# Kernel tuning notes

Measured on AMD Instinct MI355X. Metric: run time of the kernel, lower is better.

Reference implementation:

```python
import jax, jax.numpy as jnp
import numpy as np

B, N_ROIS, C, H, W = 4, 180, 512, 48, 48
STRIDE = 4
EPS = 1e-5


def _pool_one(feat, roi):
    # feat: [C,H,W], roi: [4] float (y1,x1,y2,x2) in image coords
    r = roi / STRIDE
    r0 = jnp.trunc(r[0]).astype(jnp.int32)
    r1 = jnp.trunc(r[1]).astype(jnp.int32)
    r2 = jnp.ceil(r[2]).astype(jnp.int32)
    r3 = jnp.ceil(r[3]).astype(jnp.int32)
    h_size = r2 - r0 + 1
    w_size = r3 - r1 + 1
    idx2 = jnp.arange(2)
    # AdaptiveMaxPool2d region boundaries: [floor(i*s/2), ceil((i+1)*s/2))
    sh = (idx2 * h_size) // 2
    eh = ((idx2 + 1) * h_size + 1) // 2
    sw = (idx2 * w_size) // 2
    ew = ((idx2 + 1) * w_size + 1) // 2
    hh = jnp.arange(H)[None, :]
    ww = jnp.arange(W)[None, :]
    mask_h = (hh >= (r0 + sh)[:, None]) & (hh < (r0 + eh)[:, None])  # [2,H]
    mask_w = (ww >= (r1 + sw)[:, None]) & (ww < (r1 + ew)[:, None])  # [2,W]
    neg = jnp.finfo(feat.dtype).min
    # max over W within each col region -> [2(oj), C, H]
    mw = jnp.where(mask_w[:, None, None, :], feat[None], neg).max(axis=-1)
    # max over H within each row region -> [2(oi), 2(oj), C]
    p = jnp.where(mask_h[:, None, None, :], mw[None], neg).max(axis=-1)
    # torch layout: [C, oi, oj] then flatten row-major
    return jnp.transpose(p, (2, 0, 1)).reshape(-1)  # [C*4]


def _roi_pool(features, rois):
    # features: [B,C,H,W], rois: [B,N,4] -> [B,N,C*4]
    def per_roi(roi_b):  # roi_b: [B,4]
        return jax.vmap(_pool_one)(features, roi_b)  # [B, C*4]
    out = jax.lax.map(per_roi, jnp.swapaxes(rois, 0, 1))  # [N,B,C*4]
    return jnp.swapaxes(out, 0, 1)


def _bn(x, gamma, beta):
    # training-mode BatchNorm1d over [B, N_ROIS(channels), F]: stats over (B,F)
    mean = x.mean(axis=(0, 2), keepdims=True)
    var = ((x - mean) ** 2).mean(axis=(0, 2), keepdims=True)
    return (x - mean) * jax.lax.rsqrt(var + EPS) * gamma[None, :, None] + beta[None, :, None]


def setup_inputs() -> dict:
    key = jax.random.key(0)
    k1, k2, k3, k4, k5 = jax.random.split(key, 5)
    features = jax.random.normal(k1, (B, C, H, W), dtype=jnp.float32)
    max_coord = (H - 1) * STRIDE
    y = jnp.sort(jax.random.uniform(k2, (B, N_ROIS, 2), minval=0.0, maxval=max_coord), axis=-1)
    x = jnp.sort(jax.random.uniform(k3, (B, N_ROIS, 2), minval=0.0, maxval=max_coord), axis=-1)
    rois = jnp.stack([y[..., 0], x[..., 0], y[..., 1], x[..., 1]], axis=-1)  # [B,N,4]
    F_in = C * 4
    W1 = jax.random.normal(k4, (64, F_in), dtype=jnp.float32) * 0.02
    bl1 = jnp.zeros((64,), dtype=jnp.float32)
    gamma1 = jnp.ones((N_ROIS,), dtype=jnp.float32)
    beta1 = jnp.zeros((N_ROIS,), dtype=jnp.float32)
    gamma2 = jnp.ones((N_ROIS,), dtype=jnp.float32)
    beta2 = jnp.zeros((N_ROIS,), dtype=jnp.float32)
    return {"features": features, "rois": rois, "gamma1": gamma1, "beta1": beta1,
            "W1": W1, "bl1": bl1, "gamma2": gamma2, "beta2": beta2}


def reference(features, rois, gamma1, beta1, W1, bl1, gamma2, beta2):
    pooled = _roi_pool(features, rois)            # [B, 180, 2048]
    x = jax.nn.relu(pooled)
    x = _bn(x, gamma1, beta1)
    y = jnp.einsum('bnf,of->bno', x, W1) + bl1    # [B, 180, 64]
    y = _bn(y, gamma2, beta2)
    return y
```

## Files before the change

kernel.cpp:

```cpp
#include <hip/hip_runtime.h>
#include <hip/hip_bf16.h>
#include <cfloat>
#include <math.h>

#define BB 4
#define NR 180
#define CC 512
#define HH 48
#define WW 48
#define FF (CC*4)
#define OO 64
#define EPSV 1e-5f
#define TW_LEVEL ((size_t)BB*HH*WW*CC)


typedef unsigned short us2 __attribute__((ext_vector_type(2)));

__device__ __forceinline__ unsigned pmax(unsigned a, unsigned b) {
    return __builtin_bit_cast(unsigned, __builtin_elementwise_max(
        __builtin_bit_cast(us2, a), __builtin_bit_cast(us2, b)));
}
__device__ __forceinline__ uint4 pmax4(uint4 a, uint4 b) {
    return make_uint4(pmax(a.x,b.x), pmax(a.y,b.y), pmax(a.z,b.z), pmax(a.w,b.w));
}
__device__ __forceinline__ unsigned mapb(float f) {
    unsigned fu = __float_as_uint(f);
    unsigned u = fu >> 16;
    return (fu >> 31) ? (~u & 0xFFFFu) : (u | 0x8000u);
}
__device__ __forceinline__ void unmap2(unsigned m, float& lo, float& hi) {
    unsigned t = ((~m) >> 15) & 0x00010001u;
    unsigned u = m ^ (0x80008000u ^ (t * 0x7FFFu));
    lo = __uint_as_float(u << 16);
    hi = __uint_as_float(u & 0xffff0000u);
}

__global__ __launch_bounds__(256) void k_prep(const float* __restrict__ feat,
                                              const float* __restrict__ W1,
                                              ushort* __restrict__ featB,
                                              float* __restrict__ W1T4) {
    __shared__ float tile[32][33];
    int t = threadIdx.x;
    int z = blockIdx.z;

    if (z < 4) {
        const int S = HH * WW;
        int b  = z;
        int s0 = blockIdx.x * 32;
        int c0 = blockIdx.y * 32;
        const float* src = feat + (size_t)b * CC * S;
        ushort* dst = featB + (size_t)b * S * CC;

        int cl = t >> 3;
        int sx = (t & 7) << 2;
        float4 v = *(const float4*)(src + (size_t)(c0 + cl) * S + s0 + sx);
        tile[cl][sx] = v.x; tile[cl][sx+1] = v.y; tile[cl][sx+2] = v.z; tile[cl][sx+3] = v.w;
        __syncthreads();

        int sl = t >> 3;
        int c4 = (t & 7) << 2;
        unsigned u0 = mapb(tile[c4][sl])   | (mapb(tile[c4+1][sl]) << 16);
        unsigned u1 = mapb(tile[c4+2][sl]) | (mapb(tile[c4+3][sl]) << 16);
        *(uint2*)(dst + (size_t)(s0 + sl) * CC + c0 + c4) = make_uint2(u0, u1);
    } else {
        if (blockIdx.x >= 8) return;
        int kt = blockIdx.y * 8 + blockIdx.x;
        int k0 = (kt >> 1) * 32, o0 = (kt & 1) * 32;
        int tx = t & 31, ty = t >> 5;
        #pragma unroll
        for (int k = 0; k < 4; k++) {
            int row = ty + k * 8;
            tile[row][tx] = W1[(size_t)(o0 + row) * FF + (k0 + tx)];
        }
        __syncthreads();
        #pragma unroll
        for (int k = 0; k < 4; k++) {
            int row = ty + k * 8;
            int kk = k0 + row;
            int o  = o0 + tx;
            W1T4[(size_t)(kk >> 2) * 256 + o * 4 + (kk & 3)] = tile[tx][row];
        }
    }
}

__global__ __launch_bounds__(256) void k_tab(const ushort* __restrict__ featB,
                                             ushort* __restrict__ Tw) {
    __shared__ uint4 A[WW][64];
    int by = blockIdx.x;
    int b = by / HH, y = by % HH;
    int t = threadIdx.x;
    const uint4* src = (const uint4*)(featB + (size_t)((b * HH + y) * WW) * CC);

    #pragma unroll
    for (int i = 0; i < 12; i++) {
        int it = t + i * 256;
        A[it >> 6][it & 63] = src[it];
    }
    __syncthreads();

    for (int k = 1; k <= 3; k++) {
        int h = 1 << (k - 1);
        uint4 v[12];
        #pragma unroll
        for (int i = 0; i < 12; i++) {
            int it = t + i * 256;
            int x = it >> 6, c = it & 63;
            v[i] = pmax4(A[x][c], A[min(x + h, WW - 1)][c]);
        }
        __syncthreads();
        if (k >= 2) {
            uint4* dst = (uint4*)(Tw + ((size_t)(k - 2) * BB * HH + b * HH + y) * (size_t)(WW * CC));
            #pragma unroll
            for (int i = 0; i < 12; i++) {
                int it = t + i * 256;
                A[it >> 6][it & 63] = v[i];
                dst[it] = v[i];
            }
        } else {
            #pragma unroll
            for (int i = 0; i < 12; i++) {
                int it = t + i * 256;
                A[it >> 6][it & 63] = v[i];
            }
        }
        __syncthreads();
    }
}

__global__ __launch_bounds__(1024) void k_pg(const ushort* __restrict__ featB,
                                             const ushort* __restrict__ Tw,
                                             const float* __restrict__ rois,
                                             const float* __restrict__ W1T4,
                                             const float* __restrict__ bl1,
                                             const float* __restrict__ g1,
                                             const float* __restrict__ b1,
                                             const float* __restrict__ g2,
                                             const float* __restrict__ b2,
                                             float* __restrict__ out) {
    __shared__ unsigned lu[BB][4][16][65];
    __shared__ float xs[BB][FF];
    __shared__ float pd[16][BB][OO];
    __shared__ float pw[16][OO];
    __shared__ float part_s[16], part_q[16];
    __shared__ float sm2[4], sq2[4];

    int n = blockIdx.x;
    int tid = threadIdx.x;
    int b  = tid >> 8;
    int g  = (tid >> 6) & 3;
    int c  = tid & 63;

    const float* roi = rois + ((size_t)b * NR + n) * 4;
    int r0 = (int)(roi[0] * 0.25f);
    int r1 = (int)(roi[1] * 0.25f);
    int r2 = (int)ceilf(roi[2] * 0.25f);
    int r3 = (int)ceilf(roi[3] * 0.25f);
    int hs  = r2 - r0 + 1;
    int wsz = r3 - r1 + 1;
    int eh0 = (hs + 1) >> 1, sh1 = hs >> 1;
    int sw1 = wsz >> 1;

    int len = (wsz + 1) >> 1;
    int ks  = (len >= 8) ? 3 : ((len >= 4) ? 2 : 0);
    int w   = 1 << ks;
    bool n3 = (len > 2 * w);
    int xboff = (len >> 1) - (w >> 1);
    int x0a = r1,        x0c = r1 + len - w,  x0b = r1 + xboff;
    int x1a = r1 + sw1,  x1c = r1 + wsz - w,  x1b = r1 + sw1 + xboff;
    const ushort* base = (ks == 0) ? featB : (Tw + (size_t)(ks - 2) * TW_LEVEL);

    const uint4 Z = make_uint4(0,0,0,0);
    uint4 q00 = Z, q01 = Z, q10 = Z, q11 = Z;
    for (int L = g; L < hs; L += 4) {
        size_t rowoff = (size_t)((b * HH + r0 + L) * WW) * CC;
        const uint4* p = (const uint4*)(base + rowoff) + c;
        uint4 cm0 = pmax4(p[(size_t)64 * x0a], p[(size_t)64 * x0c]);
        uint4 cm1 = pmax4(p[(size_t)64 * x1a], p[(size_t)64 * x1c]);
        if (n3) {
            cm0 = pmax4(cm0, p[(size_t)64 * x0b]);
            cm1 = pmax4(cm1, p[(size_t)64 * x1b]);
        }
        if (L <  eh0) { q00 = pmax4(q00, cm0); q01 = pmax4(q01, cm1); }
        if (L >= sh1) { q10 = pmax4(q10, cm0); q11 = pmax4(q11, cm1); }
    }

    {
        unsigned* L0 = &lu[b][g][0][c];
        unsigned a, p2;
        a = q00.x; p2 = q01.x;
        L0[ 0*65] = (a & 0xFFFFu) | (p2 << 16);
        L0[ 2*65] = (a >> 16)     | (p2 & 0xFFFF0000u);
        a = q10.x; p2 = q11.x;
        L0[ 1*65] = (a & 0xFFFFu) | (p2 << 16);
        L0[ 3*65] = (a >> 16)     | (p2 & 0xFFFF0000u);
        a = q00.y; p2 = q01.y;
        L0[ 4*65] = (a & 0xFFFFu) | (p2 << 16);
        L0[ 6*65] = (a >> 16)     | (p2 & 0xFFFF0000u);
        a = q10.y; p2 = q11.y;
        L0[ 5*65] = (a & 0xFFFFu) | (p2 << 16);
        L0[ 7*65] = (a >> 16)     | (p2 & 0xFFFF0000u);
        a = q00.z; p2 = q01.z;
        L0[ 8*65] = (a & 0xFFFFu) | (p2 << 16);
        L0[10*65] = (a >> 16)     | (p2 & 0xFFFF0000u);
        a = q10.z; p2 = q11.z;
        L0[ 9*65] = (a & 0xFFFFu) | (p2 << 16);
        L0[11*65] = (a >> 16)     | (p2 & 0xFFFF0000u);
        a = q00.w; p2 = q01.w;
        L0[12*65] = (a & 0xFFFFu) | (p2 << 16);
        L0[14*65] = (a >> 16)     | (p2 & 0xFFFF0000u);
        a = q10.w; p2 = q11.w;
        L0[13*65] = (a & 0xFFFFu) | (p2 << 16);
        L0[15*65] = (a >> 16)     | (p2 & 0xFFFF0000u);
    }
    __syncthreads();

    float s_acc = 0.f, q_acc = 0.f;
    int s  = tid & 255;
    int bb = tid >> 8;
    #pragma unroll
    for (int p = 0; p < 2; p++) {
        int fb = (p << 10) + (s << 2);
        int cc = fb >> 5;
        int j0 = (fb >> 1) & 15;
        unsigned m0 = pmax(pmax(lu[bb][0][j0  ][cc], lu[bb][1][j0  ][cc]),
                           pmax(lu[bb][2][j0  ][cc], lu[bb][3][j0  ][cc]));
        unsigned m1 = pmax(pmax(lu[bb][0][j0+1][cc], lu[bb][1][j0+1][cc]),
                           pmax(lu[bb][2][j0+1][cc], lu[bb][3][j0+1][cc]));
        m0 = pmax(m0, 0x80008000u);
        m1 = pmax(m1, 0x80008000u);
        float v0, v1, v2, v3;
        unmap2(m0, v0, v1);
        unmap2(m1, v2, v3);
        *(float4*)&xs[bb][fb] = make_float4(v0, v1, v2, v3);
        s_acc += v0 + v1 + v2 + v3;
        q_acc += v0*v0 + v1*v1 + v2*v2 + v3*v3;
    }
    for (int off = 32; off; off >>= 1) {
        s_acc += __shfl_down(s_acc, off);
        q_acc += __shfl_down(q_acc, off);
    }
    if ((tid & 63) == 0) { part_s[tid >> 6] = s_acc; part_q[tid >> 6] = q_acc; }
    __syncthreads();
    float ts = 0.f, tq = 0.f;
    #pragma unroll
    for (int i = 0; i < 16; i++) { ts += part_s[i]; tq += part_q[i]; }
    const float inv1 = 1.f / (float)(BB * FF);
    float mean = ts * inv1;
    float var  = tq * inv1 - mean * mean;
    float a1n  = g1[n] * rsqrtf(var + EPSV);
    float c1n  = b1[n] - mean * a1n;

    int sc = tid >> 6;
    int o  = tid & 63;
    int k4a = sc << 5;
    float a0 = 0.f, a1 = 0.f, a2 = 0.f, a3 = 0.f, wsum = 0.f;
    #pragma unroll 4
    for (int k4 = k4a; k4 < k4a + 32; k4++) {
        float4 w4 = *(const float4*)(W1T4 + (size_t)k4 * 256 + o * 4);
        float4 x0 = *(const float4*)&xs[0][k4 << 2];
        float4 x1 = *(const float4*)&xs[1][k4 << 2];
        float4 x2 = *(const float4*)&xs[2][k4 << 2];
        float4 x3 = *(const float4*)&xs[3][k4 << 2];
        wsum += w4.x + w4.y + w4.z + w4.w;
        a0 += w4.x*x0.x + w4.y*x0.y + w4.z*x0.z + w4.w*x0.w;
        a1 += w4.x*x1.x + w4.y*x1.y + w4.z*x1.z + w4.w*x1.w;
        a2 += w4.x*x2.x + w4.y*x2.y + w4.z*x2.z + w4.w*x2.w;
        a3 += w4.x*x3.x + w4.y*x3.y + w4.z*x3.z + w4.w*x3.w;
    }
    pd[sc][0][o] = a0; pd[sc][1][o] = a1; pd[sc][2][o] = a2; pd[sc][3][o] = a3;
    pw[sc][o] = wsum;
    __syncthreads();

    float y = 0.f;
    int bo = tid >> 6;
    if (tid < 256) {
        float dot = 0.f, wsm = 0.f;
        #pragma unroll
        for (int ss = 0; ss < 16; ss++) { dot += pd[ss][bo][o]; wsm += pw[ss][o]; }
        y = a1n * dot + c1n * wsm + bl1[o];
        float rs = y, rq = y * y;
        for (int off = 32; off; off >>= 1) {
            rs += __shfl_down(rs, off);
            rq += __shfl_down(rq, off);
        }
        if (o == 0) { sm2[bo] = rs; sq2[bo] = rq; }
    }
    __syncthreads();
    if (tid < 256) {
        float sm  = sm2[0] + sm2[1] + sm2[2] + sm2[3];
        float sqm = sq2[0] + sq2[1] + sq2[2] + sq2[3];
        const float inv2 = 1.f / 256.f;
        float mean2 = sm * inv2;
        float var2  = sqm * inv2 - mean2 * mean2;
        float r2s = rsqrtf(var2 + EPSV);
        out[((size_t)bo * NR + n) * OO + o] = (y - mean2) * r2s * g2[n] + b2[n];
    }
}

extern "C" void kernel_launch(void* const* d_in, const int* in_sizes, int n_in,
                              void* d_out, int out_size, void* d_ws, size_t ws_size,
                              hipStream_t stream) {
    const float* feat = (const float*)d_in[0];
    const float* rois = (const float*)d_in[1];
    const float* g1   = (const float*)d_in[2];
    const float* b1   = (const float*)d_in[3];
    const float* W1   = (const float*)d_in[4];
    const float* bl1  = (const float*)d_in[5];
    const float* g2   = (const float*)d_in[6];
    const float* b2   = (const float*)d_in[7];
    float* out = (float*)d_out;

    ushort* featB = (ushort*)d_ws;
    float*  W1T4  = (float*)(featB + (size_t)BB*HH*WW*CC);
    ushort* Tw    = (ushort*)(W1T4 + (size_t)OO*FF);

    k_prep<<<dim3(72, 16, 5), 256, 0, stream>>>(feat, W1, featB, W1T4);
    k_tab<<<dim3(BB * HH), 256, 0, stream>>>(featB, Tw);
    k_pg<<<dim3(NR), 1024, 0, stream>>>(featB, Tw, rois, W1T4, bl1, g1, b1, g2, b2, out);
}
```

Before: 110.4 us.

## Fuse prep, table and pooling kernels into one persistent kernel with grid barriers

Replaces the three launches (layout/bf16 conversion with W1 transpose, the sliding-max table build, and pooling plus linear plus BN) with one persistent 192-block kernel. Phases are separated by a software grid barrier built from per-block flag slots in the workspace, and shared memory is unioned across phases. This removes inter-kernel launch gaps and tail drain. In exchange, the prep phase has far fewer blocks, all blocks must be co-resident, and the barrier flags are never reset. A later call in the same workspace could therefore pass both barriers without waiting.

```diff
diff --git a/kernel.cpp b/kernel.cpp
--- a/kernel.cpp
+++ b/kernel.cpp
@@ -12,6 +12,9 @@
 #define OO 64
 #define EPSV 1e-5f
 #define TW_LEVEL ((size_t)BB*HH*WW*CC)
+#define NBLK 192
+#define MAGIC1 0xA5C3F00Du
+#define MAGIC2 0x5A3CF11Eu
 
 
 typedef unsigned short us2 __attribute__((ext_vector_type(2)));
@@ -35,117 +38,145 @@
     hi = __uint_as_float(u & 0xffff0000u);
 }
 
-__global__ __launch_bounds__(256) void k_prep(const float* __restrict__ feat,
-                                              const float* __restrict__ W1,
-                                              ushort* __restrict__ featB,
-                                              float* __restrict__ W1T4) {
-    __shared__ float tile[32][33];
-    int t = threadIdx.x;
-    int z = blockIdx.z;
-
-    if (z < 4) {
+union SmemT {
+    float tileA[4][32][33];
+    uint4 rowA[WW][64];
+    struct {
+        unsigned lu[BB][4][16][65];
+        float xs[BB][FF];
+        float pd[16][BB][OO];
+        float pw[16][OO];
+        float part_s[16], part_q[16];
+        float sm2[4], sq2[4];
+    } pg;
+};
+
+__device__ __forceinline__ void grid_barrier(unsigned* slots, unsigned magic,
+                                             int bid, int tid) {
+    __syncthreads();
+    if (tid == 0) {
+        __threadfence();
+        __hip_atomic_store(slots + bid, magic, __ATOMIC_RELEASE,
+                           __HIP_MEMORY_SCOPE_AGENT);
+    }
+    if (tid < NBLK) {
+        while (__hip_atomic_load(slots + tid, __ATOMIC_RELAXED,
+                                 __HIP_MEMORY_SCOPE_AGENT) != magic)
+            __builtin_amdgcn_s_sleep(1);
+    }
+    __syncthreads();
+    __threadfence();
+}
+
+__global__ __launch_bounds__(1024) void k_fused(
+        const float* __restrict__ feat, const float* __restrict__ rois,
+        const float* __restrict__ W1,
+        ushort* __restrict__ featB, float* __restrict__ W1T4,
+        ushort* __restrict__ Tw, unsigned* __restrict__ bar,
+        const float* __restrict__ bl1,
+        const float* __restrict__ g1, const float* __restrict__ b1,
+        const float* __restrict__ g2, const float* __restrict__ b2,
+        float* __restrict__ out) {
+    __shared__ SmemT sm;
+    int bid = blockIdx.x;
+    int tid = threadIdx.x;
+
+    {
+        int sub = tid >> 8;
+        int t   = tid & 255;
+        float (*tile)[33] = sm.tileA[sub];
         const int S = HH * WW;
-        int b  = z;
-        int s0 = blockIdx.x * 32;
-        int c0 = blockIdx.y * 32;
-        const float* src = feat + (size_t)b * CC * S;
-        ushort* dst = featB + (size_t)b * S * CC;
-
-        int cl = t >> 3;
-        int sx = (t & 7) << 2;
-        float4 v = *(const float4*)(src + (size_t)(c0 + cl) * S + s0 + sx);
-        tile[cl][sx] = v.x; tile[cl][sx+1] = v.y; tile[cl][sx+2] = v.z; tile[cl][sx+3] = v.w;
+        #pragma unroll 1
+        for (int i = 0; i < 6; i++) {
+            int u   = (bid * 4 + sub) * 6 + i;
+            int b   = u / 1152;
+            int rem = u - b * 1152;
+            int c0  = (rem / 72) * 32;
+            int s0  = (rem % 72) * 32;
+            const float* src = feat + (size_t)b * CC * S;
+            ushort* dst = featB + (size_t)b * S * CC;
+
+            int cl = t >> 3;
+            int sx = (t & 7) << 2;
+            float4 v = *(const float4*)(src + (size_t)(c0 + cl) * S + s0 + sx);
+            tile[cl][sx] = v.x; tile[cl][sx+1] = v.y;
+            tile[cl][sx+2] = v.z; tile[cl][sx+3] = v.w;
+            __syncthreads();
+            int sl = t >> 3;
+            int c4 = (t & 7) << 2;
+            unsigned u0 = mapb(tile[c4][sl])   | (mapb(tile[c4+1][sl]) << 16);
+            unsigned u1 = mapb(tile[c4+2][sl]) | (mapb(tile[c4+3][sl]) << 16);
+            *(uint2*)(dst + (size_t)(s0 + sl) * CC + c0 + c4) = make_uint2(u0, u1);
+            __syncthreads();
+        }
+        if (bid >= 184) {
+            #pragma unroll 1
+            for (int j = 0; j < 4; j++) {
+                int kt = (bid - 184) * 16 + sub * 4 + j;
+                int k0 = (kt >> 1) * 32, o0 = (kt & 1) * 32;
+                int tx = t & 31, ty = t >> 5;
+                #pragma unroll
+                for (int k = 0; k < 4; k++) {
+                    int row = ty + k * 8;
+                    tile[row][tx] = W1[(size_t)(o0 + row) * FF + (k0 + tx)];
+                }
+                __syncthreads();
+                #pragma unroll
+                for (int k = 0; k < 4; k++) {
+                    int row = ty + k * 8;
+                    int kk = k0 + row;
+                    int o  = o0 + tx;
+                    W1T4[(size_t)(kk >> 2) * 256 + o * 4 + (kk & 3)] = tile[tx][row];
+                }
+                __syncthreads();
+            }
+        }
+    }
+
+    grid_barrier(bar, MAGIC1, bid, tid);
+
+    {
+        int b = bid / HH, y = bid - b * HH;
+        const uint4* src = (const uint4*)(featB + (size_t)((b * HH + y) * WW) * CC);
+        #pragma unroll
+        for (int i = 0; i < 3; i++) {
+            int it = tid + i * 1024;
+            sm.rowA[it >> 6][it & 63] = src[it];
+        }
         __syncthreads();
-
-        int sl = t >> 3;
-        int c4 = (t & 7) << 2;
-        unsigned u0 = mapb(tile[c4][sl])   | (mapb(tile[c4+1][sl]) << 16);
-        unsigned u1 = mapb(tile[c4+2][sl]) | (mapb(tile[c4+3][sl]) << 16);
-        *(uint2*)(dst + (size_t)(s0 + sl) * CC + c0 + c4) = make_uint2(u0, u1);
-    } else {
-        if (blockIdx.x >= 8) return;
-        int kt = blockIdx.y * 8 + blockIdx.x;
-        int k0 = (kt >> 1) * 32, o0 = (kt & 1) * 32;
-        int tx = t & 31, ty = t >> 5;
-        #pragma unroll
-        for (int k = 0; k < 4; k++) {
-            int row = ty + k * 8;
-            tile[row][tx] = W1[(size_t)(o0 + row) * FF + (k0 + tx)];
-        }
-        __syncthreads();
-        #pragma unroll
-        for (int k = 0; k < 4; k++) {
-            int row = ty + k * 8;
-            int kk = k0 + row;
-            int o  = o0 + tx;
-            W1T4[(size_t)(kk >> 2) * 256 + o * 4 + (kk & 3)] = tile[tx][row];
-        }
-    }
-}
-
-__global__ __launch_bounds__(256) void k_tab(const ushort* __restrict__ featB,
-                                             ushort* __restrict__ Tw) {
-    __shared__ uint4 A[WW][64];
-    int by = blockIdx.x;
-    int b = by / HH, y = by % HH;
-    int t = threadIdx.x;
-    const uint4* src = (const uint4*)(featB + (size_t)((b * HH + y) * WW) * CC);
-
-    #pragma unroll
-    for (int i = 0; i < 12; i++) {
-        int it = t + i * 256;
-        A[it >> 6][it & 63] = src[it];
-    }
-    __syncthreads();
-
-    for (int k = 1; k <= 3; k++) {
-        int h = 1 << (k - 1);
-        uint4 v[12];
-        #pragma unroll
-        for (int i = 0; i < 12; i++) {
-            int it = t + i * 256;
-            int x = it >> 6, c = it & 63;
-            v[i] = pmax4(A[x][c], A[min(x + h, WW - 1)][c]);
-        }
-        __syncthreads();
-        if (k >= 2) {
-            uint4* dst = (uint4*)(Tw + ((size_t)(k - 2) * BB * HH + b * HH + y) * (size_t)(WW * CC));
+        for (int k = 1; k <= 3; k++) {
+            int h = 1 << (k - 1);
+            uint4 v[3];
             #pragma unroll
-            for (int i = 0; i < 12; i++) {
-                int it = t + i * 256;
-                A[it >> 6][it & 63] = v[i];
-                dst[it] = v[i];
+            for (int i = 0; i < 3; i++) {
+                int it = tid + i * 1024;
+                int x = it >> 6, c = it & 63;
+                v[i] = pmax4(sm.rowA[x][c], sm.rowA[min(x + h, WW - 1)][c]);
             }
-        } else {
-            #pragma unroll
-            for (int i = 0; i < 12; i++) {
-                int it = t + i * 256;
-                A[it >> 6][it & 63] = v[i];
+            __syncthreads();
+            if (k >= 2) {
+                uint4* dst = (uint4*)(Tw + ((size_t)(k - 2) * BB * HH + b * HH + y) * (size_t)(WW * CC));
+                #pragma unroll
+                for (int i = 0; i < 3; i++) {
+                    int it = tid + i * 1024;
+                    sm.rowA[it >> 6][it & 63] = v[i];
+                    dst[it] = v[i];
+                }
+            } else {
+                #pragma unroll
+                for (int i = 0; i < 3; i++) {
+                    int it = tid + i * 1024;
+                    sm.rowA[it >> 6][it & 63] = v[i];
+                }
             }
-        }
-        __syncthreads();
-    }
-}
-
-__global__ __launch_bounds__(1024) void k_pg(const ushort* __restrict__ featB,
-                                             const ushort* __restrict__ Tw,
-                                             const float* __restrict__ rois,
-                                             const float* __restrict__ W1T4,
-                                             const float* __restrict__ bl1,
-                                             const float* __restrict__ g1,
-                                             const float* __restrict__ b1,
-                                             const float* __restrict__ g2,
-                                             const float* __restrict__ b2,
-                                             float* __restrict__ out) {
-    __shared__ unsigned lu[BB][4][16][65];
-    __shared__ float xs[BB][FF];
-    __shared__ float pd[16][BB][OO];
-    __shared__ float pw[16][OO];
-    __shared__ float part_s[16], part_q[16];
-    __shared__ float sm2[4], sq2[4];
-
-    int n = blockIdx.x;
-    int tid = threadIdx.x;
+            __syncthreads();
+        }
+    }
+
+    grid_barrier(bar + 256, MAGIC2, bid, tid);
+    if (bid >= NR) return;
+
+    int n = bid;
     int b  = tid >> 8;
     int g  = (tid >> 6) & 3;
     int c  = tid & 63;
@@ -185,7 +216,7 @@
     }
 
     {
-        unsigned* L0 = &lu[b][g][0][c];
+        unsigned* L0 = &sm.pg.lu[b][g][0][c];
         unsigned a, p2;
         a = q00.x; p2 = q01.x;
         L0[ 0*65] = (a & 0xFFFFu) | (p2 << 16);
@@ -222,16 +253,16 @@
         int fb = (p << 10) + (s << 2);
         int cc = fb >> 5;
         int j0 = (fb >> 1) & 15;
-        unsigned m0 = pmax(pmax(lu[bb][0][j0  ][cc], lu[bb][1][j0  ][cc]),
-                           pmax(lu[bb][2][j0  ][cc], lu[bb][3][j0  ][cc]));
-        unsigned m1 = pmax(pmax(lu[bb][0][j0+1][cc], lu[bb][1][j0+1][cc]),
-                           pmax(lu[bb][2][j0+1][cc], lu[bb][3][j0+1][cc]));
+        unsigned m0 = pmax(pmax(sm.pg.lu[bb][0][j0  ][cc], sm.pg.lu[bb][1][j0  ][cc]),
+                           pmax(sm.pg.lu[bb][2][j0  ][cc], sm.pg.lu[bb][3][j0  ][cc]));
+        unsigned m1 = pmax(pmax(sm.pg.lu[bb][0][j0+1][cc], sm.pg.lu[bb][1][j0+1][cc]),
+                           pmax(sm.pg.lu[bb][2][j0+1][cc], sm.pg.lu[bb][3][j0+1][cc]));
         m0 = pmax(m0, 0x80008000u);
         m1 = pmax(m1, 0x80008000u);
         float v0, v1, v2, v3;
         unmap2(m0, v0, v1);
         unmap2(m1, v2, v3);
-        *(float4*)&xs[bb][fb] = make_float4(v0, v1, v2, v3);
+        *(float4*)&sm.pg.xs[bb][fb] = make_float4(v0, v1, v2, v3);
         s_acc += v0 + v1 + v2 + v3;
         q_acc += v0*v0 + v1*v1 + v2*v2 + v3*v3;
     }
@@ -239,11 +270,11 @@
         s_acc += __shfl_down(s_acc, off);
         q_acc += __shfl_down(q_acc, off);
     }
-    if ((tid & 63) == 0) { part_s[tid >> 6] = s_acc; part_q[tid >> 6] = q_acc; }
+    if ((tid & 63) == 0) { sm.pg.part_s[tid >> 6] = s_acc; sm.pg.part_q[tid >> 6] = q_acc; }
     __syncthreads();
     float ts = 0.f, tq = 0.f;
     #pragma unroll
-    for (int i = 0; i < 16; i++) { ts += part_s[i]; tq += part_q[i]; }
+    for (int i = 0; i < 16; i++) { ts += sm.pg.part_s[i]; tq += sm.pg.part_q[i]; }
     const float inv1 = 1.f / (float)(BB * FF);
     float mean = ts * inv1;
     float var  = tq * inv1 - mean * mean;
@@ -257,18 +288,19 @@
     #pragma unroll 4
     for (int k4 = k4a; k4 < k4a + 32; k4++) {
         float4 w4 = *(const float4*)(W1T4 + (size_t)k4 * 256 + o * 4);
-        float4 x0 = *(const float4*)&xs[0][k4 << 2];
-        float4 x1 = *(const float4*)&xs[1][k4 << 2];
-        float4 x2 = *(const float4*)&xs[2][k4 << 2];
-        float4 x3 = *(const float4*)&xs[3][k4 << 2];
+        float4 x0 = *(const float4*)&sm.pg.xs[0][k4 << 2];
+        float4 x1 = *(const float4*)&sm.pg.xs[1][k4 << 2];
+        float4 x2 = *(const float4*)&sm.pg.xs[2][k4 << 2];
+        float4 x3 = *(const float4*)&sm.pg.xs[3][k4 << 2];
         wsum += w4.x + w4.y + w4.z + w4.w;
         a0 += w4.x*x0.x + w4.y*x0.y + w4.z*x0.z + w4.w*x0.w;
         a1 += w4.x*x1.x + w4.y*x1.y + w4.z*x1.z + w4.w*x1.w;
         a2 += w4.x*x2.x + w4.y*x2.y + w4.z*x2.z + w4.w*x2.w;
         a3 += w4.x*x3.x + w4.y*x3.y + w4.z*x3.z + w4.w*x3.w;
     }
-    pd[sc][0][o] = a0; pd[sc][1][o] = a1; pd[sc][2][o] = a2; pd[sc][3][o] = a3;
-    pw[sc][o] = wsum;
+    sm.pg.pd[sc][0][o] = a0; sm.pg.pd[sc][1][o] = a1;
+    sm.pg.pd[sc][2][o] = a2; sm.pg.pd[sc][3][o] = a3;
+    sm.pg.pw[sc][o] = wsum;
     __syncthreads();
 
     float y = 0.f;
@@ -276,21 +308,21 @@
     if (tid < 256) {
         float dot = 0.f, wsm = 0.f;
         #pragma unroll
-        for (int ss = 0; ss < 16; ss++) { dot += pd[ss][bo][o]; wsm += pw[ss][o]; }
+        for (int ss = 0; ss < 16; ss++) { dot += sm.pg.pd[ss][bo][o]; wsm += sm.pg.pw[ss][o]; }
         y = a1n * dot + c1n * wsm + bl1[o];
         float rs = y, rq = y * y;
         for (int off = 32; off; off >>= 1) {
             rs += __shfl_down(rs, off);
             rq += __shfl_down(rq, off);
         }
-        if (o == 0) { sm2[bo] = rs; sq2[bo] = rq; }
+        if (o == 0) { sm.pg.sm2[bo] = rs; sm.pg.sq2[bo] = rq; }
     }
     __syncthreads();
     if (tid < 256) {
-        float sm  = sm2[0] + sm2[1] + sm2[2] + sm2[3];
-        float sqm = sq2[0] + sq2[1] + sq2[2] + sq2[3];
+        float smv = sm.pg.sm2[0] + sm.pg.sm2[1] + sm.pg.sm2[2] + sm.pg.sm2[3];
+        float sqm = sm.pg.sq2[0] + sm.pg.sq2[1] + sm.pg.sq2[2] + sm.pg.sq2[3];
         const float inv2 = 1.f / 256.f;
-        float mean2 = sm * inv2;
+        float mean2 = smv * inv2;
         float var2  = sqm * inv2 - mean2 * mean2;
         float r2s = rsqrtf(var2 + EPSV);
         out[((size_t)bo * NR + n) * OO + o] = (y - mean2) * r2s * g2[n] + b2[n];
@@ -311,10 +343,10 @@
     float* out = (float*)d_out;
 
     ushort* featB = (ushort*)d_ws;
-    float*  W1T4  = (float*)(featB + (size_t)BB*HH*WW*CC);
+    float*  W1T4  = (float*)(featB + TW_LEVEL);
     ushort* Tw    = (ushort*)(W1T4 + (size_t)OO*FF);
-
-    k_prep<<<dim3(72, 16, 5), 256, 0, stream>>>(feat, W1, featB, W1T4);
-    k_tab<<<dim3(BB * HH), 256, 0, stream>>>(featB, Tw);
-    k_pg<<<dim3(NR), 1024, 0, stream>>>(featB, Tw, rois, W1T4, bl1, g1, b1, g2, b2, out);
-}
+    unsigned* bar = (unsigned*)(Tw + 2 * TW_LEVEL);
+
+    k_fused<<<dim3(NBLK), 1024, 0, stream>>>(feat, rois, W1, featB, W1T4, Tw,
+                                             bar, bl1, g1, b1, g2, b2, out);
+}
```

After: 225.3 us. +104.2%, slower.

## Fuse bf16 transpose and sparse-table construction into one prep kernel

Applied to the files above, without the earlier changes.

Merges the feature transpose/bf16-key conversion kernel and the row max sparse-table kernel into a single kernel. Each block loads 64 channels of one feature row, builds the packed keys and the width-2/4/8 max levels in shared memory, and writes featB and both Tw levels directly, so featB is no longer re-read from global memory. This also removes one launch. In exchange, the kernel does more shared-memory index arithmetic and half-word packed edge handling, and the transposed writes are narrow uint2 stores.

```diff
diff --git a/kernel.cpp b/kernel.cpp
--- a/kernel.cpp
+++ b/kernel.cpp
@@ -34,37 +34,24 @@
     lo = __uint_as_float(u << 16);
     hi = __uint_as_float(u & 0xffff0000u);
 }
-
-__global__ __launch_bounds__(256) void k_prep(const float* __restrict__ feat,
-                                              const float* __restrict__ W1,
-                                              ushort* __restrict__ featB,
-                                              float* __restrict__ W1T4) {
-    __shared__ float tile[32][33];
+__device__ __forceinline__ unsigned duphi(unsigned a) {
+    return (a >> 16) | (a & 0xFFFF0000u);
+}
+
+__global__ __launch_bounds__(256) void k_prepab(const float* __restrict__ feat,
+                                                const float* __restrict__ W1,
+                                                ushort* __restrict__ featB,
+                                                float* __restrict__ W1T4,
+                                                ushort* __restrict__ Tw) {
+    __shared__ unsigned Mx[64][26];
+    __shared__ unsigned Px[64][26];
+    __shared__ unsigned Qx[64][26];
+    int bid = blockIdx.x;
     int t = threadIdx.x;
-    int z = blockIdx.z;
-
-    if (z < 4) {
-        const int S = HH * WW;
-        int b  = z;
-        int s0 = blockIdx.x * 32;
-        int c0 = blockIdx.y * 32;
-        const float* src = feat + (size_t)b * CC * S;
-        ushort* dst = featB + (size_t)b * S * CC;
-
-        int cl = t >> 3;
-        int sx = (t & 7) << 2;
-        float4 v = *(const float4*)(src + (size_t)(c0 + cl) * S + s0 + sx);
-        tile[cl][sx] = v.x; tile[cl][sx+1] = v.y; tile[cl][sx+2] = v.z; tile[cl][sx+3] = v.w;
-        __syncthreads();
-
-        int sl = t >> 3;
-        int c4 = (t & 7) << 2;
-        unsigned u0 = mapb(tile[c4][sl])   | (mapb(tile[c4+1][sl]) << 16);
-        unsigned u1 = mapb(tile[c4+2][sl]) | (mapb(tile[c4+3][sl]) << 16);
-        *(uint2*)(dst + (size_t)(s0 + sl) * CC + c0 + c4) = make_uint2(u0, u1);
-    } else {
-        if (blockIdx.x >= 8) return;
-        int kt = blockIdx.y * 8 + blockIdx.x;
+
+    if (bid >= 1536) {
+        float (*tile)[33] = (float(*)[33])&Mx[0][0];
+        int kt = bid - 1536;
         int k0 = (kt >> 1) * 32, o0 = (kt & 1) * 32;
         int tx = t & 31, ty = t >> 5;
         #pragma unroll
@@ -80,50 +67,104 @@
             int o  = o0 + tx;
             W1T4[(size_t)(kk >> 2) * 256 + o * 4 + (kk & 3)] = tile[tx][row];
         }
-    }
-}
-
-__global__ __launch_bounds__(256) void k_tab(const ushort* __restrict__ featB,
-                                             ushort* __restrict__ Tw) {
-    __shared__ uint4 A[WW][64];
-    int by = blockIdx.x;
-    int b = by / HH, y = by % HH;
-    int t = threadIdx.x;
-    const uint4* src = (const uint4*)(featB + (size_t)((b * HH + y) * WW) * CC);
-
-    #pragma unroll
-    for (int i = 0; i < 12; i++) {
-        int it = t + i * 256;
-        A[it >> 6][it & 63] = src[it];
-    }
-    __syncthreads();
-
-    for (int k = 1; k <= 3; k++) {
-        int h = 1 << (k - 1);
-        uint4 v[12];
-        #pragma unroll
-        for (int i = 0; i < 12; i++) {
-            int it = t + i * 256;
-            int x = it >> 6, c = it & 63;
-            v[i] = pmax4(A[x][c], A[min(x + h, WW - 1)][c]);
-        }
-        __syncthreads();
-        if (k >= 2) {
-            uint4* dst = (uint4*)(Tw + ((size_t)(k - 2) * BB * HH + b * HH + y) * (size_t)(WW * CC));
-            #pragma unroll
-            for (int i = 0; i < 12; i++) {
-                int it = t + i * 256;
-                A[it >> 6][it & 63] = v[i];
-                dst[it] = v[i];
-            }
-        } else {
-            #pragma unroll
-            for (int i = 0; i < 12; i++) {
-                int it = t + i * 256;
-                A[it >> 6][it & 63] = v[i];
-            }
-        }
-        __syncthreads();
+        return;
+    }
+
+    int b   = bid >> 7;
+    b = bid / 384;
+    int rem = bid - b * 384;
+    int y   = rem >> 3;
+    int c0  = (rem & 7) << 6;
+    const float* src = feat + ((size_t)(b * CC + c0) * HH + y) * WW;
+    size_t srow = ((size_t)b * HH + y) * WW;
+
+    #pragma unroll
+    for (int i = 0; i < 3; i++) {
+        int u  = t + (i << 8);
+        int cc = u / 12;
+        int xq = u - cc * 12;
+        float4 v = *(const float4*)(src + (size_t)cc * (HH * WW) + (xq << 2));
+        unsigned m01 = mapb(v.x) | (mapb(v.y) << 16);
+        unsigned m23 = mapb(v.z) | (mapb(v.w) << 16);
+        *(uint2*)&Mx[cc][xq << 1] = make_uint2(m01, m23);
+    }
+    __syncthreads();
+
+    #pragma unroll
+    for (int i = 0; i < 6; i++) {
+        int u  = t + (i << 8);
+        int ch = u / 24;
+        int xu = u - ch * 24;
+        unsigned A = Mx[ch][xu];
+        unsigned B = Mx[ch][min(xu + 1, 23)];
+        unsigned Be = (xu < 23) ? B : (A >> 16);
+        unsigned C = (A >> 16) | (Be << 16);
+        Px[ch][xu] = pmax(A, C);
+    }
+    {
+        const ushort* M16 = (const ushort*)&Mx[0][0];
+        #pragma unroll
+        for (int i = 0; i < 3; i++) {
+            int u = t + (i << 8);
+            int x = u >> 4;
+            int q = u & 15;
+            int e = (q << 2) * 52 + x;
+            unsigned h0 = M16[e], h1 = M16[e + 52], h2 = M16[e + 104], h3 = M16[e + 156];
+            *(uint2*)(featB + (srow + x) * CC + c0 + (q << 2)) =
+                make_uint2(h0 | (h1 << 16), h2 | (h3 << 16));
+        }
+    }
+    __syncthreads();
+
+    #pragma unroll
+    for (int i = 0; i < 6; i++) {
+        int u  = t + (i << 8);
+        int ch = u / 24;
+        int xu = u - ch * 24;
+        unsigned A = Px[ch][xu];
+        unsigned B = Px[ch][min(xu + 1, 23)];
+        unsigned S = (xu < 23) ? B : duphi(B);
+        Qx[ch][xu] = pmax(A, S);
+    }
+    __syncthreads();
+
+    #pragma unroll
+    for (int i = 0; i < 6; i++) {
+        int u  = t + (i << 8);
+        int ch = u / 24;
+        int xu = u - ch * 24;
+        unsigned A = Qx[ch][xu];
+        unsigned B = Qx[ch][min(xu + 2, 23)];
+        unsigned S = (xu < 22) ? B : duphi(Qx[ch][23]);
+        Mx[ch][xu] = pmax(A, S);
+    }
+    {
+        const ushort* Q16 = (const ushort*)&Qx[0][0];
+        #pragma unroll
+        for (int i = 0; i < 3; i++) {
+            int u = t + (i << 8);
+            int x = u >> 4;
+            int q = u & 15;
+            int e = (q << 2) * 52 + x;
+            unsigned h0 = Q16[e], h1 = Q16[e + 52], h2 = Q16[e + 104], h3 = Q16[e + 156];
+            *(uint2*)(Tw + srow * CC + x * CC + c0 + (q << 2)) =
+                make_uint2(h0 | (h1 << 16), h2 | (h3 << 16));
+        }
+    }
+    __syncthreads();
+
+    {
+        const ushort* L16 = (const ushort*)&Mx[0][0];
+        #pragma unroll
+        for (int i = 0; i < 3; i++) {
+            int u = t + (i << 8);
+            int x = u >> 4;
+            int q = u & 15;
+            int e = (q << 2) * 52 + x;
+            unsigned h0 = L16[e], h1 = L16[e + 52], h2 = L16[e + 104], h3 = L16[e + 156];
+            *(uint2*)(Tw + TW_LEVEL + srow * CC + x * CC + c0 + (q << 2)) =
+                make_uint2(h0 | (h1 << 16), h2 | (h3 << 16));
+        }
     }
 }
 
@@ -311,10 +352,9 @@
     float* out = (float*)d_out;
 
     ushort* featB = (ushort*)d_ws;
-    float*  W1T4  = (float*)(featB + (size_t)BB*HH*WW*CC);
+    float*  W1T4  = (float*)(featB + TW_LEVEL);
     ushort* Tw    = (ushort*)(W1T4 + (size_t)OO*FF);
 
-    k_prep<<<dim3(72, 16, 5), 256, 0, stream>>>(feat, W1, featB, W1T4);
-    k_tab<<<dim3(BB * HH), 256, 0, stream>>>(featB, Tw);
-    k_pg<<<dim3(NR), 1024, 0, stream>>>(featB, Tw, rois, W1T4, bl1, g1, b1, g2, b2, out);
-}
+    k_prepab<<<dim3(1664), 256, 0, stream>>>(feat, W1, featB, W1T4, Tw);
+    k_pg<<<NR, 1024, 0, stream>>>(featB, Tw, rois, W1T4, bl1, g1, b1, g2, b2, out);
+}
```

After: 110.3 us. Within noise of the previous version (-0.0%).
